# Optimization experiments

Measured on AMD Instinct MI355X. Metric: run time of the kernel, lower is better.

## Reference

```python
import jax, jax.numpy as jnp
import numpy as np

B, L, D, H = 4, 2048, 1024, 16
HD = D // H
NEG = -1e9  # stands in for -inf in masks; identical softmax result, grad-safe
EPS = 1e-5


def _layer_norm(x, g, b):
    mu = jnp.mean(x, axis=-1, keepdims=True)
    var = jnp.mean((x - mu) ** 2, axis=-1, keepdims=True)
    return (x - mu) * jax.lax.rsqrt(var + EPS) * g + b


def setup_inputs() -> dict:
    key = jax.random.key(0)
    ks = jax.random.split(key, 8)
    x = jax.random.normal(ks[0], (B, L, D), dtype=jnp.float32)
    # length-based padding: valid lengths in [L//2, L]; True = padded position
    lengths = jax.random.randint(ks[1], (B,), L // 2, L + 1)
    padding_mask = jnp.arange(L)[None, :] >= lengths[:, None]  # (B, L) bool
    # additive causal mask: 0 on/below diagonal, NEG above
    causal_mask = jnp.where(jnp.tril(jnp.ones((L, L), dtype=bool)), 0.0, NEG).astype(jnp.float32)

    def linear_params(k, fan_in, fan_out):
        bound = float(np.sqrt(6.0 / (fan_in + fan_out)))  # xavier_uniform
        W = jax.random.uniform(k, (fan_out, fan_in), jnp.float32, -bound, bound)
        b = jnp.zeros((fan_out,), jnp.float32)
        return W, b

    Wq, bq = linear_params(ks[2], D, D)
    Wk, bk = linear_params(ks[3], D, D)
    Wv, bv = linear_params(ks[4], D, D)
    Wo, bo = linear_params(ks[5], D, D)
    g_pre = jnp.ones((D,), jnp.float32); b_pre = jnp.zeros((D,), jnp.float32)
    g_ln = jnp.ones((D,), jnp.float32); b_ln = jnp.zeros((D,), jnp.float32)
    return {
        "x": x, "padding_mask": padding_mask, "causal_mask": causal_mask,
        "Wq": Wq, "bq": bq, "Wk": Wk, "bk": bk, "Wv": Wv, "bv": bv,
        "Wo": Wo, "bo": bo, "g_pre": g_pre, "b_pre": b_pre,
        "g_ln": g_ln, "b_ln": b_ln,
    }


def reference(x, padding_mask, causal_mask, Wq, bq, Wk, bk, Wv, bv, Wo, bo,
              g_pre, b_pre, g_ln, b_ln):
    # pre-LayerNorm (residual uses the normed x, matching the torch code)
    h = _layer_norm(x, g_pre, b_pre)  # (B, L, D)

    def heads(W, b):
        y = jnp.einsum('bld,ed->ble', h, W) + b           # torch Linear: x @ W.T + b
        return y.reshape(B, L, H, HD).transpose(0, 2, 1, 3)  # (B, H, L, HD)

    q, k, v = heads(Wq, bq), heads(Wk, bk), heads(Wv, bv)

    scores = jnp.einsum('bhld,bhmd->bhlm', q, k) / jnp.sqrt(jnp.float32(HD))
    scores = scores + causal_mask  # additive causal mask broadcast over (B, H)
    # padding mask: True = masked key position
    scores = jnp.where(padding_mask[:, None, None, :], NEG, scores)
    attn = jax.nn.softmax(scores, axis=-1)  # dropout p=0.0 (eval / disabled)

    out = jnp.einsum('bhlm,bhmd->bhld', attn, v)          # (B, H, L, HD)
    out = out.transpose(0, 2, 1, 3).reshape(B, L, D)
    out = jnp.einsum('bld,ed->ble', out, Wo) + bo
    return _layer_norm(out + h, g_ln, b_ln)
```

## Files before the change

### kernel.cpp

```cpp
#include <hip/hip_runtime.h>


#define Bq 4
#define Lq 2048
#define Dq 1024
#define Hq 16
#define HDq 64
#define Mq (Bq * Lq)

typedef __attribute__((ext_vector_type(8))) short short8;
typedef __attribute__((ext_vector_type(4))) float f32x4;
typedef __attribute__((address_space(3))) unsigned char lds_byte;
typedef __attribute__((address_space(1))) unsigned char gbl_byte;

__device__ __forceinline__ unsigned short f2b(float f) {
    unsigned int u = __float_as_uint(f);
    unsigned int r = (u + 0x7fffu + ((u >> 16) & 1u)) >> 16;
    return (unsigned short)r;
}
__device__ __forceinline__ float b2f(unsigned short u) {
    return __uint_as_float(((unsigned int)u) << 16);
}
__device__ __forceinline__ unsigned int packbf(float lo, float hi) {
    return (unsigned int)f2b(lo) | ((unsigned int)f2b(hi) << 16);
}

#define GLL16(gsrc, ldst)                                              \
    __builtin_amdgcn_global_load_lds((const gbl_byte*)(gsrc),          \
                                     (lds_byte*)(ldst), 16, 0, 0)

#define MFMA_BF16(A, B, C) \
    __builtin_amdgcn_mfma_f32_16x16x32_bf16((A), (B), (C), 0, 0, 0)

__global__ void setup_kernel(const unsigned char* __restrict__ m8,
                             int* __restrict__ lengths) {
    __shared__ int bad;
    __shared__ int fo[4];
    const int tid = threadIdx.x;
    if (tid == 0) bad = 0;
    if (tid < 4) fo[tid] = Lq;
    __syncthreads();
    for (int i = tid; i < Bq * Lq; i += 256) {
        unsigned char v = m8[i];
        if (v) {
            int r = i >> 11, c = i & (Lq - 1);
            atomicMin(&fo[r], c);
            if (c < Lq / 2) atomicOr(&bad, 1);
            else if (c < Lq - 1 && m8[i + 1] == 0) atomicOr(&bad, 1);
        }
    }
    __syncthreads();
    int anyone = (fo[0] < Lq) | (fo[1] < Lq) | (fo[2] < Lq) | (fo[3] < Lq);
    bool use8 = (bad == 0) && anyone;
    if (!use8) {
        __syncthreads();
        if (tid < 4) fo[tid] = Lq;
        __syncthreads();
        const int* m32 = (const int*)m8;
        for (int i = tid; i < Bq * Lq; i += 256) {
            if (m32[i] != 0) atomicMin(&fo[i >> 11], i & (Lq - 1));
        }
        __syncthreads();
    }
    if (tid < 4) lengths[tid] = fo[tid];
}

__global__ __launch_bounds__(256) void cvt4_kernel(
    const float* __restrict__ s0, const float* __restrict__ s1,
    const float* __restrict__ s2, const float* __restrict__ s3,
    unsigned short* __restrict__ dst) {
    const int region = blockIdx.x >> 10;
    const int i = (blockIdx.x & 1023) * 256 + threadIdx.x;
    const float* src = (region == 0) ? s0 : (region == 1) ? s1
                       : (region == 2) ? s2 : s3;
    float4 v = ((const float4*)src)[i];
    ushort4 o;
    o.x = f2b(v.x); o.y = f2b(v.y); o.z = f2b(v.z); o.w = f2b(v.w);
    ((ushort4*)dst)[(size_t)region * (Dq * Dq / 4) + i] = o;
}

__global__ __launch_bounds__(256) void ln_pre_kernel(
    const float* __restrict__ x, const float* __restrict__ g,
    const float* __restrict__ bb, unsigned short* __restrict__ out) {
    const int row = blockIdx.x, tid = threadIdx.x;
    float4 u = ((const float4*)x)[(size_t)row * 256 + tid];
    float s = u.x + u.y + u.z + u.w;
    float ss = u.x * u.x + u.y * u.y + u.z * u.z + u.w * u.w;
#pragma unroll
    for (int off = 32; off > 0; off >>= 1) {
        s += __shfl_xor(s, off);
        ss += __shfl_xor(ss, off);
    }
    __shared__ float sred[4], ssred[4];
    const int w = tid >> 6, lane = tid & 63;
    if (lane == 0) { sred[w] = s; ssred[w] = ss; }
    __syncthreads();
    s = sred[0] + sred[1] + sred[2] + sred[3];
    ss = ssred[0] + ssred[1] + ssred[2] + ssred[3];
    const float mean = s * (1.f / Dq);
    const float rstd = rsqrtf(ss * (1.f / Dq) - mean * mean + 1e-5f);
    float4 gv = ((const float4*)g)[tid];
    float4 bv = ((const float4*)bb)[tid];
    ushort4 o;
    o.x = f2b((u.x - mean) * rstd * gv.x + bv.x);
    o.y = f2b((u.y - mean) * rstd * gv.y + bv.y);
    o.z = f2b((u.z - mean) * rstd * gv.z + bv.z);
    o.w = f2b((u.w - mean) * rstd * gv.w + bv.w);
    ((ushort4*)out)[(size_t)row * 256 + tid] = o;
}

__global__ __launch_bounds__(256) void qkv_gemm_kernel(
    const unsigned short* __restrict__ A, const unsigned short* __restrict__ W3,
    const float* __restrict__ bq, const float* __restrict__ bk,
    const float* __restrict__ bv, unsigned short* __restrict__ Qo,
    unsigned short* __restrict__ Ko, unsigned short* __restrict__ Vto) {
    __shared__ unsigned short As[2][128][32];
    __shared__ unsigned short Bs[2][128][32];
    const int tid = threadIdx.x;
    const int w = tid >> 6, lane = tid & 63;
    const int lm = lane & 15, lq = lane >> 4;
    const int lin = blockIdx.y * 24 + blockIdx.x;
    const int swz = (lin & 7) * (1536 / 8) + (lin >> 3);
    const int m0 = (swz / 24) << 7, n0 = (swz % 24) << 7;
    const int wm = (w >> 1) << 6, wn = (w & 1) << 6;
    f32x4 acc[4][4];
#pragma unroll
    for (int i = 0; i < 4; ++i)
#pragma unroll
        for (int j = 0; j < 4; ++j) acc[i][j] = (f32x4){0.f, 0.f, 0.f, 0.f};

#define QKV_STAGE(BUF, K0)                                              \
    {                                                                   \
        _Pragma("unroll")                                               \
        for (int j = 0; j < 2; ++j) {                                   \
            const int base = j * 256 + w * 64;                          \
            const int slot = base + lane;                               \
            const int row = slot >> 2, c = slot & 3;                    \
            GLL16(A + (size_t)(m0 + row) * Dq + (K0) + c * 8,           \
                  (unsigned short*)As[BUF] + base * 8);                 \
            GLL16(W3 + (size_t)(n0 + row) * Dq + (K0) + c * 8,          \
                  (unsigned short*)Bs[BUF] + base * 8);                 \
        }                                                               \
    }

    QKV_STAGE(0, 0);
    __syncthreads();
    for (int k0 = 0; k0 < Dq; k0 += 32) {
        const int cur = (k0 >> 5) & 1;
        if (k0 + 32 < Dq) QKV_STAGE(cur ^ 1, k0 + 32);
        short8 af[4], bf[4];
#pragma unroll
        for (int t = 0; t < 4; ++t)
            af[t] = *(const short8*)&As[cur][wm + t * 16 + lm][lq * 8];
#pragma unroll
        for (int t = 0; t < 4; ++t)
            bf[t] = *(const short8*)&Bs[cur][wn + t * 16 + lm][lq * 8];
#pragma unroll
        for (int mt = 0; mt < 4; ++mt)
#pragma unroll
            for (int nt = 0; nt < 4; ++nt)
                acc[mt][nt] = __builtin_amdgcn_mfma_f32_16x16x32_bf16(
                    af[mt], bf[nt], acc[mt][nt], 0, 0, 0);
        __syncthreads();
    }
#undef QKV_STAGE
    const int region = n0 >> 10;
    const float* bias = (region == 0) ? bq : (region == 1) ? bk : bv;
    const float scale = (region == 0) ? 0.125f : 1.0f;
    const int nb = n0 & 1023;
#pragma unroll
    for (int nt = 0; nt < 4; ++nt) {
        const int colb = nb + wn + nt * 16 + lm;
        const float bval = bias[colb];
#pragma unroll
        for (int mt = 0; mt < 4; ++mt) {
            const int row0 = m0 + wm + mt * 16 + lq * 4;
            const int bidx = row0 >> 11, l0r = row0 & (Lq - 1);
            if (region < 2) {
                unsigned short* dst = (region == 0) ? Qo : Ko;
#pragma unroll
                for (int r = 0; r < 4; ++r)
                    dst[((size_t)(bidx * Hq + (colb >> 6)) * Lq + l0r + r) *
                            HDq + (colb & 63)] =
                        f2b((acc[mt][nt][r] + bval) * scale);
            } else {
                ushort4 o;
                o.x = f2b(acc[mt][nt][0] + bval);
                o.y = f2b(acc[mt][nt][1] + bval);
                o.z = f2b(acc[mt][nt][2] + bval);
                o.w = f2b(acc[mt][nt][3] + bval);
                *(ushort4*)&Vto[((size_t)(bidx * Hq + (colb >> 6)) * HDq +
                                 (colb & 63)) * Lq + l0r] = o;
            }
        }
    }
}

__global__ __launch_bounds__(256) void proj_gemm_kernel(
    const unsigned short* __restrict__ A, const unsigned short* __restrict__ Bw,
    const float* __restrict__ bias, float* __restrict__ Cout) {
    __shared__ unsigned short As[2][128][32];
    __shared__ unsigned short Bs[2][128][32];
    const int tid = threadIdx.x;
    const int w = tid >> 6, lane = tid & 63;
    const int lm = lane & 15, lq = lane >> 4;
    const int lin = blockIdx.y * 8 + blockIdx.x;
    const int swz = (lin & 7) * (512 / 8) + (lin >> 3);
    const int m0 = (swz >> 3) << 7, n0 = (swz & 7) << 7;
    const int wm = (w >> 1) << 6, wn = (w & 1) << 6;
    f32x4 acc[4][4];
#pragma unroll
    for (int i = 0; i < 4; ++i)
#pragma unroll
        for (int j = 0; j < 4; ++j) acc[i][j] = (f32x4){0.f, 0.f, 0.f, 0.f};

#define PROJ_STAGE(BUF, K0)                                             \
    {                                                                   \
        _Pragma("unroll")                                               \
        for (int j = 0; j < 2; ++j) {                                   \
            const int base = j * 256 + w * 64;                          \
            const int slot = base + lane;                               \
            const int row = slot >> 2, c = slot & 3;                    \
            const int rr = m0 + row, kk = (K0) + c * 8;                 \
            GLL16(A + ((size_t)((rr >> 11) * Hq + (kk >> 6)) * Lq +     \
                       (rr & (Lq - 1))) * HDq + (kk & 63),              \
                  (unsigned short*)As[BUF] + base * 8);                 \
            GLL16(Bw + (size_t)(n0 + row) * Dq + (K0) + c * 8,          \
                  (unsigned short*)Bs[BUF] + base * 8);                 \
        }                                                               \
    }

    PROJ_STAGE(0, 0);
    __syncthreads();
    for (int k0 = 0; k0 < Dq; k0 += 32) {
        const int cur = (k0 >> 5) & 1;
        if (k0 + 32 < Dq) PROJ_STAGE(cur ^ 1, k0 + 32);
        short8 af[4], bf[4];
#pragma unroll
        for (int t = 0; t < 4; ++t)
            af[t] = *(const short8*)&As[cur][wm + t * 16 + lm][lq * 8];
#pragma unroll
        for (int t = 0; t < 4; ++t)
            bf[t] = *(const short8*)&Bs[cur][wn + t * 16 + lm][lq * 8];
#pragma unroll
        for (int mt = 0; mt < 4; ++mt)
#pragma unroll
            for (int nt = 0; nt < 4; ++nt)
                acc[mt][nt] = __builtin_amdgcn_mfma_f32_16x16x32_bf16(
                    af[mt], bf[nt], acc[mt][nt], 0, 0, 0);
        __syncthreads();
    }
#undef PROJ_STAGE
#pragma unroll
    for (int nt = 0; nt < 4; ++nt) {
        const float bval = bias[n0 + wn + nt * 16 + lm];
#pragma unroll
        for (int mt = 0; mt < 4; ++mt)
#pragma unroll
            for (int r = 0; r < 4; ++r)
                Cout[(size_t)(m0 + wm + mt * 16 + lq * 4 + r) * Dq + n0 + wn +
                     nt * 16 + lm] = acc[mt][nt][r] + bval;
    }
}

__global__ __launch_bounds__(256, 2) void attn_kernel(
    const unsigned short* __restrict__ Qg, const unsigned short* __restrict__ Kg,
    const unsigned short* __restrict__ Vtg, const int* __restrict__ lengths,
    unsigned short* __restrict__ Og) {
    __shared__ unsigned short Kbuf[2][4096];
    __shared__ unsigned short Vbuf[2][4096];
    __shared__ unsigned short Ps[4][2][16][72];
    const int lin = blockIdx.x + (blockIdx.y << 3) + (blockIdx.z << 7);
    const int xcd = lin & 7, sidx = lin >> 3;
    const int grp = xcd * 8 + (sidx & 7);
    const int bx = sidx >> 3;
    const int hh = grp & 15, b = grp >> 4;
    const int tid = threadIdx.x, w = tid >> 6, lane = tid & 63;
    const int lm = lane & 15, lq = lane >> 4;
    const int len = lengths[b];
    const int mxk = (len + 63) >> 6;
    const size_t hb = (size_t)(b * Hq + hh) * Lq * HDq;
    const unsigned short* Vb = Vtg + hb;

    const int srow = w * 8 + (lane >> 3);
    const int ssw = (lane & 7) ^ (lane >> 3);
    const unsigned short* pK = Kg + hb + (size_t)srow * HDq + ssw * 8;
    const unsigned short* pV = Vb + (size_t)srow * Lq + ssw * 8;

#define STAGE_KV(BUF, KB)                                                   \
    {                                                                       \
        GLL16(pK + (size_t)(KB)*HDq, &Kbuf[(BUF)][(w * 64) * 8]);           \
        GLL16(pK + (size_t)((KB) + 32) * HDq,                               \
              &Kbuf[(BUF)][(256 + w * 64) * 8]);                            \
        GLL16(pV + (KB), &Vbuf[(BUF)][(w * 64) * 8]);                       \
        GLL16(pV + (size_t)32 * Lq + (KB),                                  \
              &Vbuf[(BUF)][(256 + w * 64) * 8]);                            \
    }

#pragma unroll
    for (int pass = 0; pass < 2; ++pass) {
        const int qt = pass ? bx : (15 - bx);
        const int l0 = qt << 7;
        short8 qf[2][2];
#pragma unroll
        for (int s = 0; s < 2; ++s)
#pragma unroll
            for (int h = 0; h < 2; ++h)
                qf[s][h] = *(const short8*)(Qg + hb +
                    (size_t)(l0 + w * 32 + s * 16 + lm) * HDq + h * 32 + lq * 8);
        f32x4 oacc[2][4];
        float m_i[2], l_i[2];
#pragma unroll
        for (int s = 0; s < 2; ++s) {
            m_i[s] = -1e30f; l_i[s] = 0.f;
#pragma unroll
            for (int t = 0; t < 4; ++t)
                oacc[s][t] = (f32x4){0.f, 0.f, 0.f, 0.f};
        }
        int nkt = 2 * qt + 2;
        if (nkt > mxk) nkt = mxk;
        STAGE_KV(0, 0);
        __syncthreads();
        for (int kt = 0; kt < nkt; ++kt) {
            const int kb = kt << 6;
            const int cur = kt & 1;
            if (kt + 1 < nkt) STAGE_KV(cur ^ 1, (kt + 1) << 6);
            short8 kf[4][2], vf[4][2];
#pragma unroll
            for (int t = 0; t < 4; ++t) {
                const int ro = (t * 16 + lm) * 64;
                const int sx = lm & 7;
#pragma unroll
                for (int h = 0; h < 2; ++h) {
                    const int off = ro + (((h * 4 + lq) ^ sx) << 3);
                    kf[t][h] = *(const short8*)&Kbuf[cur][off];
                    vf[t][h] = *(const short8*)&Vbuf[cur][off];
                }
            }
            f32x4 sc[2][4];
            __builtin_amdgcn_s_setprio(1);
#pragma unroll
            for (int s = 0; s < 2; ++s) {
#pragma unroll
                for (int t = 0; t < 4; ++t) {
                    f32x4 z = (f32x4){0.f, 0.f, 0.f, 0.f};
                    z = MFMA_BF16(kf[t][0], qf[s][0], z);
                    z = MFMA_BF16(kf[t][1], qf[s][1], z);
                    sc[s][t] = z;
                }
            }
            __builtin_amdgcn_s_setprio(0);
#pragma unroll
            for (int s = 0; s < 2; ++s) {
                const int qmin = l0 + w * 32 + s * 16;
                float pvv[16];
                float mx = -1e30f;
                if ((kb + 63 <= qmin) && (kb + 63 < len)) {
#pragma unroll
                    for (int i = 0; i < 16; ++i) {
                        const float v = sc[s][i >> 2][i & 3];
                        pvv[i] = v;
                        mx = fmaxf(mx, v);
                    }
                } else {
                    const int qq = qmin + lm;
#pragma unroll
                    for (int t = 0; t < 4; ++t)
#pragma unroll
                        for (int r = 0; r < 4; ++r) {
                            const int key = kb + t * 16 + lq * 4 + r;
                            float v = sc[s][t][r];
                            if (key > qq || key >= len) v = -1e30f;
                            pvv[t * 4 + r] = v;
                            mx = fmaxf(mx, v);
                        }
                }
                mx = fmaxf(mx, __shfl_xor(mx, 16));
                mx = fmaxf(mx, __shfl_xor(mx, 32));
                const float mnew = fmaxf(m_i[s], mx);
                float psum = 0.f;
#pragma unroll
                for (int i = 0; i < 16; ++i) {
                    const float p = __expf(pvv[i] - mnew);
                    pvv[i] = p;
                    psum += p;
                }
#pragma unroll
                for (int t = 0; t < 4; ++t) {
                    uint2 uu;
                    uu.x = packbf(pvv[t * 4 + 0], pvv[t * 4 + 1]);
                    uu.y = packbf(pvv[t * 4 + 2], pvv[t * 4 + 3]);
                    *(uint2*)&Ps[w][s][lm][t * 16 + lq * 4] = uu;
                }
                psum += __shfl_xor(psum, 16);
                psum += __shfl_xor(psum, 32);
                const float alpha = __expf(m_i[s] - mnew);
                m_i[s] = mnew;
                l_i[s] = l_i[s] * alpha + psum;
#pragma unroll
                for (int t = 0; t < 4; ++t) {
                    oacc[s][t][0] *= alpha; oacc[s][t][1] *= alpha;
                    oacc[s][t][2] *= alpha; oacc[s][t][3] *= alpha;
                }
            }
            asm volatile("s_waitcnt lgkmcnt(0)" ::: "memory");
            __builtin_amdgcn_s_setprio(1);
#pragma unroll
            for (int s = 0; s < 2; ++s) {
                short8 pf0 = *(const short8*)&Ps[w][s][lm][lq * 8];
                short8 pf1 = *(const short8*)&Ps[w][s][lm][32 + lq * 8];
#pragma unroll
                for (int t = 0; t < 4; ++t) {
                    oacc[s][t] = MFMA_BF16(vf[t][0], pf0, oacc[s][t]);
                    oacc[s][t] = MFMA_BF16(vf[t][1], pf1, oacc[s][t]);
                }
            }
            __builtin_amdgcn_s_setprio(0);
            __syncthreads();
        }
#pragma unroll
        for (int s = 0; s < 2; ++s) {
            const float inv = 1.f / l_i[s];
            unsigned short* Ot =
                Og + hb + (size_t)(l0 + w * 32 + s * 16 + lm) * HDq;
#pragma unroll
            for (int t = 0; t < 4; ++t) {
                ushort4 o;
                o.x = f2b(oacc[s][t][0] * inv);
                o.y = f2b(oacc[s][t][1] * inv);
                o.z = f2b(oacc[s][t][2] * inv);
                o.w = f2b(oacc[s][t][3] * inv);
                *(ushort4*)(Ot + t * 16 + lq * 4) = o;
            }
        }
    }
#undef STAGE_KV
}

__global__ __launch_bounds__(256) void ln_final_kernel(
    const float* __restrict__ pj, const unsigned short* __restrict__ h,
    const float* __restrict__ g, const float* __restrict__ bb,
    float* __restrict__ out) {
    const int row = blockIdx.x, tid = threadIdx.x;
    float4 a = ((const float4*)pj)[(size_t)row * 256 + tid];
    ushort4 hv = ((const ushort4*)h)[(size_t)row * 256 + tid];
    float f0 = a.x + b2f(hv.x), f1 = a.y + b2f(hv.y);
    float f2 = a.z + b2f(hv.z), f3 = a.w + b2f(hv.w);
    float s = f0 + f1 + f2 + f3;
    float ss = f0 * f0 + f1 * f1 + f2 * f2 + f3 * f3;
#pragma unroll
    for (int off = 32; off > 0; off >>= 1) {
        s += __shfl_xor(s, off);
        ss += __shfl_xor(ss, off);
    }
    __shared__ float sred[4], ssred[4];
    const int w = tid >> 6, lane = tid & 63;
    if (lane == 0) { sred[w] = s; ssred[w] = ss; }
    __syncthreads();
    s = sred[0] + sred[1] + sred[2] + sred[3];
    ss = ssred[0] + ssred[1] + ssred[2] + ssred[3];
    const float mean = s * (1.f / Dq);
    const float rstd = rsqrtf(ss * (1.f / Dq) - mean * mean + 1e-5f);
    float4 gv = ((const float4*)g)[tid];
    float4 bv = ((const float4*)bb)[tid];
    float4 o;
    o.x = (f0 - mean) * rstd * gv.x + bv.x;
    o.y = (f1 - mean) * rstd * gv.y + bv.y;
    o.z = (f2 - mean) * rstd * gv.z + bv.z;
    o.w = (f3 - mean) * rstd * gv.w + bv.w;
    ((float4*)out)[(size_t)row * 256 + tid] = o;
}

extern "C" void kernel_launch(void* const* d_in, const int* in_sizes, int n_in,
                              void* d_out, int out_size, void* d_ws,
                              size_t ws_size, hipStream_t stream) {
    const float* x = (const float*)d_in[0];
    const unsigned char* mask = (const unsigned char*)d_in[1];
    const float* Wq = (const float*)d_in[3];
    const float* bq = (const float*)d_in[4];
    const float* Wk = (const float*)d_in[5];
    const float* bk = (const float*)d_in[6];
    const float* Wv = (const float*)d_in[7];
    const float* bvv = (const float*)d_in[8];
    const float* Wo = (const float*)d_in[9];
    const float* bo = (const float*)d_in[10];
    const float* g_pre = (const float*)d_in[11];
    const float* b_pre = (const float*)d_in[12];
    const float* g_ln = (const float*)d_in[13];
    const float* b_ln = (const float*)d_in[14];

    const size_t SZ = (size_t)Mq * Dq;
    const size_t WSZ = (size_t)Dq * Dq;
    unsigned short* h = (unsigned short*)d_ws;
    unsigned short* q = h + SZ;
    unsigned short* k = q + SZ;
    unsigned short* vT = k + SZ;
    unsigned short* at = vT + SZ;
    unsigned short* W3 = at + SZ;
    unsigned short* wob = W3 + 3 * WSZ;
    float* proj = (float*)(wob + WSZ);
    int* lengths = (int*)(proj + SZ);

    setup_kernel<<<1, 256, 0, stream>>>(mask, lengths);
    cvt4_kernel<<<4096, 256, 0, stream>>>(Wq, Wk, Wv, Wo, W3);
    ln_pre_kernel<<<Mq, 256, 0, stream>>>(x, g_pre, b_pre, h);

    qkv_gemm_kernel<<<dim3(3 * Dq / 128, Mq / 128), 256, 0, stream>>>(
        h, W3, bq, bk, bvv, q, k, vT);
    attn_kernel<<<dim3(Lq / 256, Hq, Bq), 256, 0, stream>>>(q, k, vT, lengths,
                                                            at);
    proj_gemm_kernel<<<dim3(Dq / 128, Mq / 128), 256, 0, stream>>>(at, wob, bo,
                                                                   proj);
    ln_final_kernel<<<Mq, 256, 0, stream>>>(proj, h, g_ln, b_ln,
                                            (float*)d_out);
}
```

Before: 345.5 us.

## Split attention work across 8 waves of 16 rows and use exp2 softmax

The attention kernel goes from 256 to 512 threads per block. Each wave now owns 16 query rows instead of 32, so per-wave register use (scores, accumulators, Q fragments) is halved and more waves can hide latency. Each thread issues one K and one V load per tile instead of two. Separately, the log2(e) factor is folded into the Q scale in the QKV GEMM epilogue so the softmax can use exp2f instead of __expf. In exchange, every wave still reads the full K/V fragments from LDS, so LDS read traffic per unit of useful work doubles, and block-wide barriers now synchronise more waves.

```diff
diff --git a/kernel.cpp b/kernel.cpp
--- a/kernel.cpp
+++ b/kernel.cpp
@@ -166,7 +166,7 @@
 #undef QKV_STAGE
     const int region = n0 >> 10;
     const float* bias = (region == 0) ? bq : (region == 1) ? bk : bv;
-    const float scale = (region == 0) ? 0.125f : 1.0f;
+    const float scale = (region == 0) ? 0.125f * 1.4426950408889634f : 1.0f;
     const int nb = n0 & 1023;
 #pragma unroll
     for (int nt = 0; nt < 4; ++nt) {
@@ -263,13 +263,13 @@
     }
 }
 
-__global__ __launch_bounds__(256, 2) void attn_kernel(
+__global__ __launch_bounds__(512, 4) void attn_kernel(
     const unsigned short* __restrict__ Qg, const unsigned short* __restrict__ Kg,
     const unsigned short* __restrict__ Vtg, const int* __restrict__ lengths,
     unsigned short* __restrict__ Og) {
     __shared__ unsigned short Kbuf[2][4096];
     __shared__ unsigned short Vbuf[2][4096];
-    __shared__ unsigned short Ps[4][2][16][72];
+    __shared__ unsigned short Ps[8][16][72];
     const int lin = blockIdx.x + (blockIdx.y << 3) + (blockIdx.z << 7);
     const int xcd = lin & 7, sidx = lin >> 3;
     const int grp = xcd * 8 + (sidx & 7);
@@ -282,41 +282,31 @@
     const size_t hb = (size_t)(b * Hq + hh) * Lq * HDq;
     const unsigned short* Vb = Vtg + hb;
 
-    const int srow = w * 8 + (lane >> 3);
-    const int ssw = (lane & 7) ^ (lane >> 3);
+    const int srow = tid >> 3;
+    const int ssw = (tid & 7) ^ (srow & 7);
     const unsigned short* pK = Kg + hb + (size_t)srow * HDq + ssw * 8;
     const unsigned short* pV = Vb + (size_t)srow * Lq + ssw * 8;
 
 #define STAGE_KV(BUF, KB)                                                   \
     {                                                                       \
         GLL16(pK + (size_t)(KB)*HDq, &Kbuf[(BUF)][(w * 64) * 8]);           \
-        GLL16(pK + (size_t)((KB) + 32) * HDq,                               \
-              &Kbuf[(BUF)][(256 + w * 64) * 8]);                            \
         GLL16(pV + (KB), &Vbuf[(BUF)][(w * 64) * 8]);                       \
-        GLL16(pV + (size_t)32 * Lq + (KB),                                  \
-              &Vbuf[(BUF)][(256 + w * 64) * 8]);                            \
     }
 
 #pragma unroll
     for (int pass = 0; pass < 2; ++pass) {
         const int qt = pass ? bx : (15 - bx);
         const int l0 = qt << 7;
-        short8 qf[2][2];
-#pragma unroll
-        for (int s = 0; s < 2; ++s)
-#pragma unroll
-            for (int h = 0; h < 2; ++h)
-                qf[s][h] = *(const short8*)(Qg + hb +
-                    (size_t)(l0 + w * 32 + s * 16 + lm) * HDq + h * 32 + lq * 8);
-        f32x4 oacc[2][4];
-        float m_i[2], l_i[2];
-#pragma unroll
-        for (int s = 0; s < 2; ++s) {
-            m_i[s] = -1e30f; l_i[s] = 0.f;
-#pragma unroll
-            for (int t = 0; t < 4; ++t)
-                oacc[s][t] = (f32x4){0.f, 0.f, 0.f, 0.f};
-        }
+        const int r0 = l0 + w * 16;
+        short8 qf[2];
+#pragma unroll
+        for (int h = 0; h < 2; ++h)
+            qf[h] = *(const short8*)(Qg + hb + (size_t)(r0 + lm) * HDq +
+                                     h * 32 + lq * 8);
+        f32x4 oacc[4];
+        float m_i = -1e30f, l_i = 0.f;
+#pragma unroll
+        for (int t = 0; t < 4; ++t) oacc[t] = (f32x4){0.f, 0.f, 0.f, 0.f};
         int nkt = 2 * qt + 2;
         if (nkt > mxk) nkt = mxk;
         STAGE_KV(0, 0);
@@ -337,101 +327,87 @@
                     vf[t][h] = *(const short8*)&Vbuf[cur][off];
                 }
             }
-            f32x4 sc[2][4];
+            f32x4 sc[4];
             __builtin_amdgcn_s_setprio(1);
 #pragma unroll
-            for (int s = 0; s < 2; ++s) {
-#pragma unroll
-                for (int t = 0; t < 4; ++t) {
-                    f32x4 z = (f32x4){0.f, 0.f, 0.f, 0.f};
-                    z = MFMA_BF16(kf[t][0], qf[s][0], z);
-                    z = MFMA_BF16(kf[t][1], qf[s][1], z);
-                    sc[s][t] = z;
+            for (int t = 0; t < 4; ++t) {
+                f32x4 z = (f32x4){0.f, 0.f, 0.f, 0.f};
+                z = MFMA_BF16(kf[t][0], qf[0], z);
+                z = MFMA_BF16(kf[t][1], qf[1], z);
+                sc[t] = z;
+            }
+            __builtin_amdgcn_s_setprio(0);
+            float pvv[16];
+            float mx = -1e30f;
+            if ((kb + 63 <= r0) && (kb + 63 < len)) {
+#pragma unroll
+                for (int i = 0; i < 16; ++i) {
+                    const float v = sc[i >> 2][i & 3];
+                    pvv[i] = v;
+                    mx = fmaxf(mx, v);
                 }
-            }
-            __builtin_amdgcn_s_setprio(0);
-#pragma unroll
-            for (int s = 0; s < 2; ++s) {
-                const int qmin = l0 + w * 32 + s * 16;
-                float pvv[16];
-                float mx = -1e30f;
-                if ((kb + 63 <= qmin) && (kb + 63 < len)) {
-#pragma unroll
-                    for (int i = 0; i < 16; ++i) {
-                        const float v = sc[s][i >> 2][i & 3];
-                        pvv[i] = v;
+            } else {
+                const int qq = r0 + lm;
+#pragma unroll
+                for (int t = 0; t < 4; ++t)
+#pragma unroll
+                    for (int r = 0; r < 4; ++r) {
+                        const int key = kb + t * 16 + lq * 4 + r;
+                        float v = sc[t][r];
+                        if (key > qq || key >= len) v = -1e30f;
+                        pvv[t * 4 + r] = v;
                         mx = fmaxf(mx, v);
                     }
-                } else {
-                    const int qq = qmin + lm;
-#pragma unroll
-                    for (int t = 0; t < 4; ++t)
-#pragma unroll
-                        for (int r = 0; r < 4; ++r) {
-                            const int key = kb + t * 16 + lq * 4 + r;
-                            float v = sc[s][t][r];
-                            if (key > qq || key >= len) v = -1e30f;
-                            pvv[t * 4 + r] = v;
-                            mx = fmaxf(mx, v);
-                        }
-                }
-                mx = fmaxf(mx, __shfl_xor(mx, 16));
-                mx = fmaxf(mx, __shfl_xor(mx, 32));
-                const float mnew = fmaxf(m_i[s], mx);
-                float psum = 0.f;
-#pragma unroll
-                for (int i = 0; i < 16; ++i) {
-                    const float p = __expf(pvv[i] - mnew);
-                    pvv[i] = p;
-                    psum += p;
-                }
-#pragma unroll
-                for (int t = 0; t < 4; ++t) {
-                    uint2 uu;
-                    uu.x = packbf(pvv[t * 4 + 0], pvv[t * 4 + 1]);
-                    uu.y = packbf(pvv[t * 4 + 2], pvv[t * 4 + 3]);
-                    *(uint2*)&Ps[w][s][lm][t * 16 + lq * 4] = uu;
-                }
-                psum += __shfl_xor(psum, 16);
-                psum += __shfl_xor(psum, 32);
-                const float alpha = __expf(m_i[s] - mnew);
-                m_i[s] = mnew;
-                l_i[s] = l_i[s] * alpha + psum;
-#pragma unroll
-                for (int t = 0; t < 4; ++t) {
-                    oacc[s][t][0] *= alpha; oacc[s][t][1] *= alpha;
-                    oacc[s][t][2] *= alpha; oacc[s][t][3] *= alpha;
-                }
+            }
+            mx = fmaxf(mx, __shfl_xor(mx, 16));
+            mx = fmaxf(mx, __shfl_xor(mx, 32));
+            const float mnew = fmaxf(m_i, mx);
+            float psum = 0.f;
+#pragma unroll
+            for (int i = 0; i < 16; ++i) {
+                const float p = exp2f(pvv[i] - mnew);
+                pvv[i] = p;
+                psum += p;
+            }
+#pragma unroll
+            for (int t = 0; t < 4; ++t) {
+                uint2 uu;
+                uu.x = packbf(pvv[t * 4 + 0], pvv[t * 4 + 1]);
+                uu.y = packbf(pvv[t * 4 + 2], pvv[t * 4 + 3]);
+                *(uint2*)&Ps[w][lm][t * 16 + lq * 4] = uu;
+            }
+            psum += __shfl_xor(psum, 16);
+            psum += __shfl_xor(psum, 32);
+            const float alpha = exp2f(m_i - mnew);
+            m_i = mnew;
+            l_i = l_i * alpha + psum;
+#pragma unroll
+            for (int t = 0; t < 4; ++t) {
+                oacc[t][0] *= alpha; oacc[t][1] *= alpha;
+                oacc[t][2] *= alpha; oacc[t][3] *= alpha;
             }
             asm volatile("s_waitcnt lgkmcnt(0)" ::: "memory");
+            short8 pf0 = *(const short8*)&Ps[w][lm][lq * 8];
+            short8 pf1 = *(const short8*)&Ps[w][lm][32 + lq * 8];
             __builtin_amdgcn_s_setprio(1);
 #pragma unroll
-            for (int s = 0; s < 2; ++s) {
-                short8 pf0 = *(const short8*)&Ps[w][s][lm][lq * 8];
-                short8 pf1 = *(const short8*)&Ps[w][s][lm][32 + lq * 8];
-#pragma unroll
-                for (int t = 0; t < 4; ++t) {
-                    oacc[s][t] = MFMA_BF16(vf[t][0], pf0, oacc[s][t]);
-                    oacc[s][t] = MFMA_BF16(vf[t][1], pf1, oacc[s][t]);
-                }
+            for (int t = 0; t < 4; ++t) {
+                oacc[t] = MFMA_BF16(vf[t][0], pf0, oacc[t]);
+                oacc[t] = MFMA_BF16(vf[t][1], pf1, oacc[t]);
             }
             __builtin_amdgcn_s_setprio(0);
             __syncthreads();
         }
-#pragma unroll
-        for (int s = 0; s < 2; ++s) {
-            const float inv = 1.f / l_i[s];
-            unsigned short* Ot =
-                Og + hb + (size_t)(l0 + w * 32 + s * 16 + lm) * HDq;
-#pragma unroll
-            for (int t = 0; t < 4; ++t) {
-                ushort4 o;
-                o.x = f2b(oacc[s][t][0] * inv);
-                o.y = f2b(oacc[s][t][1] * inv);
-                o.z = f2b(oacc[s][t][2] * inv);
-                o.w = f2b(oacc[s][t][3] * inv);
-                *(ushort4*)(Ot + t * 16 + lq * 4) = o;
-            }
+        const float inv = 1.f / l_i;
+        unsigned short* Ot = Og + hb + (size_t)(r0 + lm) * HDq;
+#pragma unroll
+        for (int t = 0; t < 4; ++t) {
+            ushort4 o;
+            o.x = f2b(oacc[t][0] * inv);
+            o.y = f2b(oacc[t][1] * inv);
+            o.z = f2b(oacc[t][2] * inv);
+            o.w = f2b(oacc[t][3] * inv);
+            *(ushort4*)(Ot + t * 16 + lq * 4) = o;
         }
     }
 #undef STAGE_KV
@@ -507,7 +483,7 @@
 
     qkv_gemm_kernel<<<dim3(3 * Dq / 128, Mq / 128), 256, 0, stream>>>(
         h, W3, bq, bk, bvv, q, k, vT);
-    attn_kernel<<<dim3(Lq / 256, Hq, Bq), 256, 0, stream>>>(q, k, vT, lengths,
+    attn_kernel<<<dim3(Lq / 256, Hq, Bq), 512, 0, stream>>>(q, k, vT, lengths,
                                                             at);
     proj_gemm_kernel<<<dim3(Dq / 128, Mq / 128), 256, 0, stream>>>(at, wob, bo,
                                                                    proj);
```

Measured after the change: 354.0 us. +2.5%, slower.

## Stage Q/K epilogue through LDS, fold log2e into Q scale, skip redundant rescale

Applied to the files above, without the earlier changes.

The QKV GEMM epilogue for the Q and K regions now writes the tile into the reused shared buffer and then emits coalesced 16-byte row stores, replacing scattered 2-byte stores. The Q scale absorbs log2(e), so the attention softmax can use exp2f instead of __expf. The running-max rescale of the output accumulators is also skipped when no lane's max increased. These changes add an extra barrier and LDS round-trip in the GEMM epilogue and a wave-wide branch in the attention loop.

```diff
diff --git a/kernel.cpp b/kernel.cpp
--- a/kernel.cpp
+++ b/kernel.cpp
@@ -114,8 +114,7 @@
     const float* __restrict__ bq, const float* __restrict__ bk,
     const float* __restrict__ bv, unsigned short* __restrict__ Qo,
     unsigned short* __restrict__ Ko, unsigned short* __restrict__ Vto) {
-    __shared__ unsigned short As[2][128][32];
-    __shared__ unsigned short Bs[2][128][32];
+    __shared__ unsigned short SH[16384];
     const int tid = threadIdx.x;
     const int w = tid >> 6, lane = tid & 63;
     const int lm = lane & 15, lq = lane >> 4;
@@ -137,9 +136,9 @@
             const int slot = base + lane;                               \
             const int row = slot >> 2, c = slot & 3;                    \
             GLL16(A + (size_t)(m0 + row) * Dq + (K0) + c * 8,           \
-                  (unsigned short*)As[BUF] + base * 8);                 \
+                  SH + (BUF)*4096 + base * 8);                          \
             GLL16(W3 + (size_t)(n0 + row) * Dq + (K0) + c * 8,          \
-                  (unsigned short*)Bs[BUF] + base * 8);                 \
+                  SH + 8192 + (BUF)*4096 + base * 8);                   \
         }                                                               \
     }
 
@@ -151,10 +150,12 @@
         short8 af[4], bf[4];
 #pragma unroll
         for (int t = 0; t < 4; ++t)
-            af[t] = *(const short8*)&As[cur][wm + t * 16 + lm][lq * 8];
+            af[t] = *(const short8*)&SH[cur * 4096 + (wm + t * 16 + lm) * 32 +
+                                        lq * 8];
 #pragma unroll
         for (int t = 0; t < 4; ++t)
-            bf[t] = *(const short8*)&Bs[cur][wn + t * 16 + lm][lq * 8];
+            bf[t] = *(const short8*)&SH[8192 + cur * 4096 +
+                                        (wn + t * 16 + lm) * 32 + lq * 8];
 #pragma unroll
         for (int mt = 0; mt < 4; ++mt)
 #pragma unroll
@@ -166,24 +167,43 @@
 #undef QKV_STAGE
     const int region = n0 >> 10;
     const float* bias = (region == 0) ? bq : (region == 1) ? bk : bv;
-    const float scale = (region == 0) ? 0.125f : 1.0f;
+    const float scale = (region == 0) ? 0.125f * 1.4426950408889634f : 1.0f;
     const int nb = n0 & 1023;
-#pragma unroll
-    for (int nt = 0; nt < 4; ++nt) {
-        const int colb = nb + wn + nt * 16 + lm;
-        const float bval = bias[colb];
-#pragma unroll
-        for (int mt = 0; mt < 4; ++mt) {
-            const int row0 = m0 + wm + mt * 16 + lq * 4;
-            const int bidx = row0 >> 11, l0r = row0 & (Lq - 1);
-            if (region < 2) {
-                unsigned short* dst = (region == 0) ? Qo : Ko;
+    if (region < 2) {
+        unsigned short* dst = (region == 0) ? Qo : Ko;
+#pragma unroll
+        for (int nt = 0; nt < 4; ++nt) {
+            const int cl = wn + nt * 16 + lm;
+            const float bval = bias[nb + cl];
+#pragma unroll
+            for (int mt = 0; mt < 4; ++mt) {
+                const int rl = wm + mt * 16 + lq * 4;
 #pragma unroll
                 for (int r = 0; r < 4; ++r)
-                    dst[((size_t)(bidx * Hq + (colb >> 6)) * Lq + l0r + r) *
-                            HDq + (colb & 63)] =
+                    SH[(rl + r) * 128 + cl] =
                         f2b((acc[mt][nt][r] + bval) * scale);
-            } else {
+            }
+        }
+        __syncthreads();
+        const int rr = tid >> 1, cc = (tid & 1) << 6;
+        const int row0 = m0 + rr;
+        const int bidx = row0 >> 11, l0r = row0 & (Lq - 1);
+        const int head = (nb + cc) >> 6;
+        unsigned short* dbase =
+            dst + ((size_t)(bidx * Hq + head) * Lq + l0r) * HDq;
+#pragma unroll
+        for (int j = 0; j < 8; ++j)
+            *(short8*)(dbase + j * 8) =
+                *(const short8*)&SH[rr * 128 + cc + j * 8];
+    } else {
+#pragma unroll
+        for (int nt = 0; nt < 4; ++nt) {
+            const int colb = nb + wn + nt * 16 + lm;
+            const float bval = bias[colb];
+#pragma unroll
+            for (int mt = 0; mt < 4; ++mt) {
+                const int row0 = m0 + wm + mt * 16 + lq * 4;
+                const int bidx = row0 >> 11, l0r = row0 & (Lq - 1);
                 ushort4 o;
                 o.x = f2b(acc[mt][nt][0] + bval);
                 o.y = f2b(acc[mt][nt][1] + bval);
@@ -381,7 +401,7 @@
                 float psum = 0.f;
 #pragma unroll
                 for (int i = 0; i < 16; ++i) {
-                    const float p = __expf(pvv[i] - mnew);
+                    const float p = exp2f(pvv[i] - mnew);
                     pvv[i] = p;
                     psum += p;
                 }
@@ -394,14 +414,17 @@
                 }
                 psum += __shfl_xor(psum, 16);
                 psum += __shfl_xor(psum, 32);
-                const float alpha = __expf(m_i[s] - mnew);
-                m_i[s] = mnew;
-                l_i[s] = l_i[s] * alpha + psum;
-#pragma unroll
-                for (int t = 0; t < 4; ++t) {
-                    oacc[s][t][0] *= alpha; oacc[s][t][1] *= alpha;
-                    oacc[s][t][2] *= alpha; oacc[s][t][3] *= alpha;
-                }
+                if (__any(mx > m_i[s])) {
+                    const float alpha = exp2f(m_i[s] - mnew);
+                    m_i[s] = mnew;
+                    l_i[s] *= alpha;
+#pragma unroll
+                    for (int t = 0; t < 4; ++t) {
+                        oacc[s][t][0] *= alpha; oacc[s][t][1] *= alpha;
+                        oacc[s][t][2] *= alpha; oacc[s][t][3] *= alpha;
+                    }
+                }
+                l_i[s] += psum;
             }
             asm volatile("s_waitcnt lgkmcnt(0)" ::: "memory");
             __builtin_amdgcn_s_setprio(1);
```

Result: slower. 369.4 us (+6.9%).
